# Kernel tuning notes

Hardware: AMD Instinct MI355X
Metric: run time of the kernel (lower is better)

The kernel has to match this reference:

```python
import jax, jax.numpy as jnp
import numpy as np

D = 1024   # embedding_dim
H = 16     # head_num
DH = D // H
STD = 0.02


def setup_inputs() -> dict:
    key = jax.random.key(0)
    ks = jax.random.split(key, 8)
    B, S = 16, 2048
    inp = {
        "hidden_states": jax.random.normal(ks[0], (B, S, D), dtype=jnp.float32),
        "attention_mask": jnp.zeros((B, 1, S), dtype=jnp.float32),
        # nn.Linear params, stored as [in, out] for direct matmul
        "Wq": jax.random.normal(ks[1], (D, D), dtype=jnp.float32) * STD,
        "bq": jnp.zeros((D,), dtype=jnp.float32),
        "Wqa": jax.random.normal(ks[2], (D, H), dtype=jnp.float32) * STD,
        "bqa": jnp.zeros((H,), dtype=jnp.float32),
        "Wk": jax.random.normal(ks[3], (D, D), dtype=jnp.float32) * STD,
        "bk": jnp.zeros((D,), dtype=jnp.float32),
        "Wka": jax.random.normal(ks[4], (D, H), dtype=jnp.float32) * STD,
        "bka": jnp.zeros((H,), dtype=jnp.float32),
        "Wt": jax.random.normal(ks[5], (D, D), dtype=jnp.float32) * STD,
        "bt": jnp.zeros((D,), dtype=jnp.float32),
    }
    return inp


def reference(hidden_states, attention_mask, Wq, bq, Wqa, bqa, Wk, bk, Wka, bka, Wt, bt):
    B, S, _ = hidden_states.shape
    scale = 1.0 / np.sqrt(DH).astype(np.float32)

    mixed_q = hidden_states @ Wq + bq          # [B,S,D]
    mixed_k = hidden_states @ Wk + bk          # [B,S,D]

    # per-head query pooling scores: [B,S,H] -> [B,H,S]
    q_score = jnp.transpose(mixed_q @ Wqa + bqa, (0, 2, 1)) * scale + attention_mask
    q_weight = jax.nn.softmax(q_score, axis=-1)                 # [B,H,S]

    q_layer = mixed_q.reshape(B, S, H, DH).transpose(0, 2, 1, 3)  # [B,H,S,dh]
    pooled_q = jnp.einsum('bhs,bhsd->bhd', q_weight, q_layer)     # [B,H,dh]
    pooled_q_flat = pooled_q.reshape(B, 1, D)                     # [B,1,D] (head-major)

    # elementwise modulate keys with pooled query (broadcast, no repeat)
    mixed_qk = mixed_k * pooled_q_flat                            # [B,S,D]

    qk_score = jnp.transpose(mixed_qk @ Wka + bka, (0, 2, 1)) * scale + attention_mask
    qk_weight = jax.nn.softmax(qk_score, axis=-1)                 # [B,H,S]

    k_layer = mixed_qk.reshape(B, S, H, DH).transpose(0, 2, 1, 3)  # [B,H,S,dh]
    pooled_k = jnp.einsum('bhs,bhsd->bhd', qk_weight, k_layer)     # [B,H,dh]

    weighted = pooled_k[:, :, None, :] * q_layer                   # [B,H,S,dh]
    weighted = weighted.transpose(0, 2, 1, 3).reshape(B, S, D)     # [B,S,D]

    return weighted @ Wt + bt + mixed_q
```

## Files before the change

### kernel.cpp

```cpp
#include <hip/hip_runtime.h>
#include <hip/hip_bf16.h>
#include <stdint.h>

#define D_ 1024
#define H_ 16
#define DH_ 64
#define S_ 2048
#define B_ 16
static constexpr float SCALE = 0.125f;

typedef __bf16 bf16_t;
typedef __bf16 bf16x8 __attribute__((ext_vector_type(8)));
typedef __bf16 bf16x4 __attribute__((ext_vector_type(4)));
typedef float  f32x4  __attribute__((ext_vector_type(4)));

__device__ __forceinline__ void llds16(const void* g, void* l) {
  __builtin_amdgcn_global_load_lds(
      (const __attribute__((address_space(1))) void*)g,
      (__attribute__((address_space(3))) void*)l, 16, 0, 0);
}

__global__ __launch_bounds__(256)
void prep_all(const float* __restrict__ Wq, const float* __restrict__ Wk,
              const float* __restrict__ Wt, const float* __restrict__ Wqa,
              const float* __restrict__ Wka, const float* __restrict__ hs,
              bf16_t* __restrict__ WqT, bf16_t* __restrict__ WkT,
              bf16_t* __restrict__ WtT, bf16_t* __restrict__ WqaT,
              bf16_t* __restrict__ WkaT, bf16_t* __restrict__ hsb) {
  __shared__ bf16_t t[64][65];
  const int z = blockIdx.z;
  const int tid = threadIdx.x;
  if (z < 3) {
    const float* src = (z == 0) ? Wq : (z == 1) ? Wk : Wt;
    bf16_t* dst      = (z == 0) ? WqT : (z == 1) ? WkT : WtT;
    const int n0 = blockIdx.x * 64, k0 = blockIdx.y * 64;
    const int r = tid >> 4, c4 = (tid & 15) * 4;
#pragma unroll
    for (int p = 0; p < 4; ++p) {
      int row = p * 16 + r;
      f32x4 f = *(const f32x4*)&src[(size_t)(k0 + row) * 1024 + n0 + c4];
#pragma unroll
      for (int i = 0; i < 4; ++i) t[row][c4 + i] = (bf16_t)f[i];
    }
    __syncthreads();
#pragma unroll
    for (int p = 0; p < 4; ++p) {
      int row = p * 16 + r;
      bf16x4 v;
#pragma unroll
      for (int i = 0; i < 4; ++i) v[i] = t[c4 + i][row];
      *(bf16x4*)&dst[(size_t)(n0 + row) * 1024 + k0 + c4] = v;
    }
  } else if (z == 3) {
    int g = (blockIdx.y * 16 + blockIdx.x) * 256 + tid;
    if (g < 2048) {
      const float* src = (g < 1024) ? Wqa : Wka;
      bf16_t* dst      = (g < 1024) ? WqaT : WkaT;
      int k = g & 1023;
#pragma unroll
      for (int h = 0; h < H_; ++h) dst[h * 1024 + k] = (bf16_t)src[k * H_ + h];
    }
  } else {
    const int slice = z - 4;
    const int fb = blockIdx.y * 16 + blockIdx.x;
    const size_t tbase = ((size_t)slice * 256 + fb) * 256 + tid;
#pragma unroll
    for (int i = 0; i < 4; ++i) {
      size_t e = (tbase + (size_t)i * 1048576) * 8;
      f32x4 a = *(const f32x4*)&hs[e];
      f32x4 b = *(const f32x4*)&hs[e + 4];
      bf16x8 o;
#pragma unroll
      for (int j = 0; j < 4; ++j) { o[j] = (bf16_t)a[j]; o[4 + j] = (bf16_t)b[j]; }
      *(bf16x8*)&hsb[e] = o;
    }
  }
}

__global__ __launch_bounds__(512, 1)
void gemm_qk(const bf16_t* __restrict__ A, const bf16_t* __restrict__ WqT,
             const bf16_t* __restrict__ WkT, const float* __restrict__ bq,
             const float* __restrict__ bk, bf16_t* __restrict__ mq,
             bf16_t* __restrict__ mk) {
  constexpr int K = 1024, N = 1024;
  __shared__ __align__(16) bf16_t lds[2][2][2][256 * 32];
  const int tid = threadIdx.x;
  const int lane = tid & 63, wid = tid >> 6;
  const int wm = wid >> 2, wn = wid & 3;

  const int wgid = (blockIdx.x & 7) * 128 + (blockIdx.x >> 3);
  const int m0 = (wgid >> 3) * 256;
  const int nsel = wgid & 7;
  const int n0 = (nsel & 3) * 256;
  const bf16_t* BT = (nsel < 4) ? WqT : WkT;
  const float* bias = (nsel < 4) ? bq : bk;
  bf16_t* Cout = (nsel < 4) ? mq : mk;

  int srow[2], scol[2];
#pragma unroll
  for (int ld = 0; ld < 2; ++ld) {
    int c = ld * 512 + tid;
    srow[ld] = c >> 2;
    scol[ld] = (((c & 3) - (srow[ld] & 3)) & 3) * 8;
  }

  const int ar = lane & 15;
  const int kc = lane >> 4;

  f32x4 acc[8][4] = {};

#define STAGE_(MAT, KH, KOFF, NXT)                                             \
  {                                                                            \
    const bf16_t* srcb = (MAT == 0) ? A : BT;                                  \
    const int rb = (MAT == 0) ? m0 : n0;                                       \
    _Pragma("unroll")                                                          \
    for (int ld = 0; ld < 2; ++ld) {                                           \
      llds16(srcb + (size_t)(rb + srow[ld]) * K + (KOFF) + (KH) * 32 + scol[ld], \
             &lds[NXT][MAT][KH][(ld * 512 + tid) * 8]);                        \
    }                                                                          \
  }

#define COMPUTE_(KH, MH, CUR)                                                  \
  {                                                                            \
    bf16x8 af[4], bg[4];                                                       \
    _Pragma("unroll")                                                          \
    for (int mm = 0; mm < 4; ++mm) {                                           \
      int r = wm * 128 + ((MH) * 4 + mm) * 16 + ar;                            \
      int slot = (kc + (r & 3)) & 3;                                           \
      af[mm] = *(const bf16x8*)&lds[CUR][0][KH][r * 32 + slot * 8];            \
    }                                                                          \
    _Pragma("unroll")                                                          \
    for (int nn = 0; nn < 4; ++nn) {                                           \
      int r = wn * 64 + nn * 16 + ar;                                          \
      int slot = (kc + (r & 3)) & 3;                                           \
      bg[nn] = *(const bf16x8*)&lds[CUR][1][KH][r * 32 + slot * 8];            \
    }                                                                          \
    __builtin_amdgcn_s_setprio(1);                                             \
    _Pragma("unroll")                                                          \
    for (int mm = 0; mm < 4; ++mm)                                             \
      _Pragma("unroll")                                                        \
      for (int nn = 0; nn < 4; ++nn)                                           \
        acc[(MH) * 4 + mm][nn] = __builtin_amdgcn_mfma_f32_16x16x32_bf16(      \
            af[mm], bg[nn], acc[(MH) * 4 + mm][nn], 0, 0, 0);                  \
    __builtin_amdgcn_s_setprio(0);                                             \
  }

  STAGE_(0, 0, 0, 0); STAGE_(1, 0, 0, 0); STAGE_(0, 1, 0, 0); STAGE_(1, 1, 0, 0);

#pragma unroll 1
  for (int t = 0; t < 15; ++t) {
    const int cur = t & 1, nxt = cur ^ 1;
    const int koff = (t + 1) * 64;
    STAGE_(0, 0, koff, nxt);
    asm volatile("s_waitcnt vmcnt(6)" ::: "memory");
    __builtin_amdgcn_s_barrier();
    COMPUTE_(0, 0, cur);
    STAGE_(1, 0, koff, nxt);
    COMPUTE_(0, 1, cur);
    STAGE_(0, 1, koff, nxt);
    asm volatile("s_waitcnt vmcnt(6)" ::: "memory");
    __builtin_amdgcn_s_barrier();
    COMPUTE_(1, 0, cur);
    STAGE_(1, 1, koff, nxt);
    COMPUTE_(1, 1, cur);
  }
  asm volatile("s_waitcnt vmcnt(4)" ::: "memory");
  __builtin_amdgcn_s_barrier();
  COMPUTE_(0, 0, 1);
  COMPUTE_(0, 1, 1);
  asm volatile("s_waitcnt vmcnt(0)" ::: "memory");
  __builtin_amdgcn_s_barrier();
  COMPUTE_(1, 0, 1);
  COMPUTE_(1, 1, 1);
#undef STAGE_
#undef COMPUTE_

  __syncthreads();

  float* st = (float*)&lds[0][0][0][0] + wid * (16 * 68);
  const int erow = lane >> 2;
  const int ecol = (lane & 3) * 16;
  const int gcb = n0 + wn * 64;
  const int qrow = (lane >> 4) * 4;
  const int qcol = lane & 15;
  f32x4 bb[4];
#pragma unroll
  for (int q = 0; q < 4; ++q) bb[q] = *(const f32x4*)&bias[gcb + ecol + q * 4];
#pragma unroll
  for (int m = 0; m < 8; ++m) {
#pragma unroll
    for (int n = 0; n < 4; ++n)
#pragma unroll
      for (int j = 0; j < 4; ++j)
        st[(qrow + j) * 68 + n * 16 + qcol] = acc[m][n][j];
    asm volatile("s_waitcnt lgkmcnt(0)" ::: "memory");
    __builtin_amdgcn_sched_barrier(0);
    const int grow = m0 + wm * 128 + m * 16 + erow;
    f32x4 v[4];
#pragma unroll
    for (int q = 0; q < 4; ++q) v[q] = *(f32x4*)&st[erow * 68 + ecol + q * 4];
#pragma unroll
    for (int q = 0; q < 4; ++q)
#pragma unroll
      for (int i = 0; i < 4; ++i) v[q][i] += bb[q][i];
    bf16x8 o0, o1;
#pragma unroll
    for (int i = 0; i < 4; ++i) { o0[i] = (bf16_t)v[0][i]; o0[4 + i] = (bf16_t)v[1][i]; }
#pragma unroll
    for (int i = 0; i < 4; ++i) { o1[i] = (bf16_t)v[2][i]; o1[4 + i] = (bf16_t)v[3][i]; }
    bf16_t* op = Cout + (size_t)grow * N + gcb + ecol;
    *(bf16x8*)&op[0] = o0;
    *(bf16x8*)&op[8] = o1;
  }
}

__global__ __launch_bounds__(256, 2)
void gemm_out(const bf16_t* __restrict__ A, const bf16_t* __restrict__ BT,
              const float* __restrict__ bias, float* __restrict__ Cout,
              const bf16_t* __restrict__ resid, const float* __restrict__ pkA) {
  constexpr int K = 1024, N = 1024;
  __shared__ __align__(16) bf16_t lA[128 * 32];
  __shared__ __align__(16) bf16_t lB[128 * 32];
  __shared__ __align__(16) float est[4][16 * 68];
  const int tid = threadIdx.x;
  const int lane = tid & 63, wid = tid >> 6;
  const int wr = wid >> 1, wc = wid & 1;

  const int wgid = (blockIdx.x & 7) * 256 + (blockIdx.x >> 3);
  const int m0 = (wgid >> 3) * 128;
  const int n0 = (wgid & 7) * 128;
  const int b = m0 / S_;

  const int ar = lane & 15;
  const int kq = lane >> 4;

  int rowc[2], colc[2], dstoff[2];
#pragma unroll
  for (int j = 0; j < 2; ++j) {
    int c = j * 256 + tid;
    int row = c >> 2, s = c & 3;
    rowc[j] = row;
    colc[j] = (((s - (row >> 1)) & 3) << 3);
    dstoff[j] = c * 8;
  }

  f32x4 acc[4][4] = {};

  for (int k0 = 0; k0 < K; k0 += 32) {
#pragma unroll
    for (int j = 0; j < 2; ++j) {
      llds16(BT + (size_t)(n0 + rowc[j]) * K + k0 + colc[j], lB + dstoff[j]);
      bf16x8 v = *(const bf16x8*)(A + (size_t)(m0 + rowc[j]) * K + k0 + colc[j]);
      const float* pkp = pkA + b * D_ + k0 + colc[j];
      f32x4 p0 = *(const f32x4*)pkp;
      f32x4 p1 = *(const f32x4*)(pkp + 4);
      bf16x8 o;
#pragma unroll
      for (int i = 0; i < 4; ++i) {
        o[i]     = (bf16_t)((float)v[i] * p0[i]);
        o[4 + i] = (bf16_t)((float)v[4 + i] * p1[i]);
      }
      *(bf16x8*)&lA[dstoff[j]] = o;
    }
    __syncthreads();
    bf16x8 af[4], bg[4];
#pragma unroll
    for (int m = 0; m < 4; ++m) {
      int r = wr * 64 + m * 16 + ar;
      af[m] = *(const bf16x8*)&lA[r * 32 + (((kq + (r >> 1)) & 3) << 3)];
    }
#pragma unroll
    for (int n = 0; n < 4; ++n) {
      int r = wc * 64 + n * 16 + ar;
      bg[n] = *(const bf16x8*)&lB[r * 32 + (((kq + (r >> 1)) & 3) << 3)];
    }
#pragma unroll
    for (int m = 0; m < 4; ++m)
#pragma unroll
      for (int n = 0; n < 4; ++n)
        acc[m][n] = __builtin_amdgcn_mfma_f32_16x16x32_bf16(af[m], bg[n], acc[m][n], 0, 0, 0);
    __syncthreads();
  }

  float* st = est[wid];
  const int erow = lane >> 2;
  const int ecol = (lane & 3) * 16;
  const int gcb = n0 + wc * 64;
  const int qrow = (lane >> 4) * 4;
  const int qcol = lane & 15;
  f32x4 bb[4];
#pragma unroll
  for (int q = 0; q < 4; ++q) bb[q] = *(const f32x4*)&bias[gcb + ecol + q * 4];
#pragma unroll
  for (int m = 0; m < 4; ++m) {
#pragma unroll
    for (int n = 0; n < 4; ++n)
#pragma unroll
      for (int j = 0; j < 4; ++j)
        st[(qrow + j) * 68 + n * 16 + qcol] = acc[m][n][j];
    asm volatile("s_waitcnt lgkmcnt(0)" ::: "memory");
    __builtin_amdgcn_sched_barrier(0);
    const int grow = m0 + wr * 64 + m * 16 + erow;
    f32x4 v[4];
#pragma unroll
    for (int q = 0; q < 4; ++q) v[q] = *(f32x4*)&st[erow * 68 + ecol + q * 4];
#pragma unroll
    for (int q = 0; q < 4; ++q)
#pragma unroll
      for (int i = 0; i < 4; ++i) v[q][i] += bb[q][i];
    bf16x8 r0 = *(const bf16x8*)&resid[(size_t)grow * N + gcb + ecol];
    bf16x8 r1 = *(const bf16x8*)&resid[(size_t)grow * N + gcb + ecol + 8];
#pragma unroll
    for (int i = 0; i < 4; ++i) { v[0][i] += (float)r0[i]; v[1][i] += (float)r0[4 + i]; }
#pragma unroll
    for (int i = 0; i < 4; ++i) { v[2][i] += (float)r1[i]; v[3][i] += (float)r1[4 + i]; }
    float* op = Cout + (size_t)grow * N + gcb + ecol;
#pragma unroll
    for (int q = 0; q < 4; ++q) *(f32x4*)&op[q * 4] = v[q];
  }
}

template <int PER_B>
__global__ __launch_bounds__(256)
void score_kernel(const bf16_t* __restrict__ X, const bf16_t* __restrict__ WaT,
                  const float* __restrict__ ba, const float* __restrict__ mask,
                  float* __restrict__ scores) {
  const int lane = threadIdx.x & 63, wid = threadIdx.x >> 6;
  const int m0 = blockIdx.x * 64 + wid * 16;
  const int ar = lane & 15, ak = (lane >> 4) * 8;
  const int bb = m0 >> 11;
  const bf16_t* Wb = WaT + (PER_B ? (size_t)bb * H_ * D_ : 0);
  f32x4 acc = {};
  for (int k0 = 0; k0 < D_; k0 += 32) {
    bf16x8 a = *(const bf16x8*)&X[(size_t)(m0 + ar) * D_ + k0 + ak];
    bf16x8 b = *(const bf16x8*)&Wb[(size_t)ar * D_ + k0 + ak];
    acc = __builtin_amdgcn_mfma_f32_16x16x32_bf16(a, b, acc, 0, 0, 0);
  }
  const int h = lane & 15;
  const int srow = m0 + (lane >> 4) * 4;
  const int s0 = srow - bb * S_;
  const float bah = ba[h];
  f32x4 mv = *(const f32x4*)&mask[(size_t)bb * S_ + s0];
  f32x4 outv;
#pragma unroll
  for (int j = 0; j < 4; ++j)
    outv[j] = (acc[j] + bah) * SCALE + mv[j];
  *(f32x4*)&scores[((size_t)(bb * H_ + h)) * S_ + s0] = outv;
}

__global__ __launch_bounds__(256)
void softmax_rows(const float* __restrict__ scores, float* __restrict__ wout) {
  __shared__ float rA[4], rB[4];
  const int tid = threadIdx.x, lane = tid & 63, wid = tid >> 6;
  const float* srow = scores + (size_t)blockIdx.x * S_;
  float* wrow = wout + (size_t)blockIdx.x * S_;
  f32x4 v0 = *(const f32x4*)&srow[tid * 4];
  f32x4 v1 = *(const f32x4*)&srow[1024 + tid * 4];
  float mx = fmaxf(fmaxf(fmaxf(v0[0], v0[1]), fmaxf(v0[2], v0[3])),
                   fmaxf(fmaxf(v1[0], v1[1]), fmaxf(v1[2], v1[3])));
#pragma unroll
  for (int o = 32; o; o >>= 1) mx = fmaxf(mx, __shfl_xor(mx, o));
  if (lane == 0) rA[wid] = mx;
  __syncthreads();
  mx = fmaxf(fmaxf(rA[0], rA[1]), fmaxf(rA[2], rA[3]));
  float sum = 0.f;
#pragma unroll
  for (int i = 0; i < 4; ++i) { v0[i] = __expf(v0[i] - mx); sum += v0[i]; }
#pragma unroll
  for (int i = 0; i < 4; ++i) { v1[i] = __expf(v1[i] - mx); sum += v1[i]; }
#pragma unroll
  for (int o = 32; o; o >>= 1) sum += __shfl_xor(sum, o);
  if (lane == 0) rB[wid] = sum;
  __syncthreads();
  sum = rB[0] + rB[1] + rB[2] + rB[3];
  const float inv = 1.0f / sum;
#pragma unroll
  for (int i = 0; i < 4; ++i) { v0[i] *= inv; v1[i] *= inv; }
  *(f32x4*)&wrow[tid * 4] = v0;
  *(f32x4*)&wrow[1024 + tid * 4] = v1;
}

__global__ __launch_bounds__(256)
void pool_partial(const bf16_t* __restrict__ X, const float* __restrict__ w,
                  float* __restrict__ partials) {
  __shared__ float sm[2][1024];
  const int tid = threadIdx.x;
  const int chunk = blockIdx.x, b = blockIdx.y;
  const int s0 = chunk * 32;
  const int dc = (tid & 127) * 8;
  const int sp = tid >> 7;
  const int h = dc >> 6;
  const float* wrow = w + ((size_t)b * H_ + h) * S_ + s0;
  const bf16_t* Xb = X + ((size_t)b * S_ + s0) * D_ + dc;
  float acc[8] = {};
  for (int s = sp; s < 32; s += 2) {
    bf16x8 xv = *(const bf16x8*)&Xb[(size_t)s * D_];
    float wt = wrow[s];
#pragma unroll
    for (int j = 0; j < 8; ++j) acc[j] += wt * (float)xv[j];
  }
#pragma unroll
  for (int j = 0; j < 8; ++j) sm[sp][dc + j] = acc[j];
  __syncthreads();
  const int d0 = tid * 4;
  f32x4 r;
#pragma unroll
  for (int j = 0; j < 4; ++j) r[j] = sm[0][d0 + j] + sm[1][d0 + j];
  *(f32x4*)&partials[((size_t)chunk * B_ + b) * D_ + d0] = r;
}

template <int MODE>
__global__ __launch_bounds__(256)
void pool_reduce(const float* __restrict__ partials, const float* __restrict__ pq,
                 const bf16_t* __restrict__ WkaT, float* __restrict__ pooled,
                 bf16_t* __restrict__ wka_s) {
  const int idx = blockIdx.x * 256 + threadIdx.x;
  float s = 0.f;
#pragma unroll 8
  for (int c = 0; c < 64; ++c) s += partials[(size_t)c * (B_ * D_) + idx];
  if (MODE == 1) s *= pq[idx];
  pooled[idx] = s;
  if (MODE == 0) {
    const int b = idx >> 10, d = idx & 1023;
#pragma unroll
    for (int h = 0; h < H_; ++h)
      wka_s[((size_t)b * H_ + h) * D_ + d] = (bf16_t)(s * (float)WkaT[h * D_ + d]);
  }
}

extern "C" void kernel_launch(void* const* d_in, const int* in_sizes, int n_in,
                              void* d_out, int out_size, void* d_ws, size_t ws_size,
                              hipStream_t stream) {
  const float* hs   = (const float*)d_in[0];
  const float* mask = (const float*)d_in[1];
  const float* Wq   = (const float*)d_in[2];
  const float* bq   = (const float*)d_in[3];
  const float* Wqa  = (const float*)d_in[4];
  const float* bqa  = (const float*)d_in[5];
  const float* Wk   = (const float*)d_in[6];
  const float* bk   = (const float*)d_in[7];
  const float* Wka  = (const float*)d_in[8];
  const float* bka  = (const float*)d_in[9];
  const float* Wt   = (const float*)d_in[10];
  const float* bt   = (const float*)d_in[11];

  char* ws = (char*)d_ws;
  float*  pq    = (float*)(ws + (64u << 10));
  float*  pk    = (float*)(ws + (128u << 10));
  bf16_t* wka_s = (bf16_t*)(ws + (256u << 10));
  bf16_t* WqaT  = (bf16_t*)(ws + (1u << 20));
  bf16_t* WkaT  = (bf16_t*)(ws + (1u << 20) + 32768);
  bf16_t* WqT   = (bf16_t*)(ws + (2u << 20));
  bf16_t* WkT   = (bf16_t*)(ws + (4u << 20));
  bf16_t* WtT   = (bf16_t*)(ws + (6u << 20));
  bf16_t* hsb   = (bf16_t*)(ws + (8u << 20));
  bf16_t* mq    = (bf16_t*)(ws + (8u << 20) + ((size_t)64 << 20));
  bf16_t* mk    = (bf16_t*)(ws + (8u << 20) + ((size_t)128 << 20));
  float* scores = (float*)(ws + (8u << 20) + ((size_t)192 << 20));
  float* wsm    = (float*)(ws + (8u << 20) + ((size_t)194 << 20));
  float* parts  = (float*)(ws + (8u << 20) + ((size_t)196 << 20));

  prep_all<<<dim3(16, 16, 20), 256, 0, stream>>>(Wq, Wk, Wt, Wqa, Wka, hs,
                                                 WqT, WkT, WtT, WqaT, WkaT, hsb);

  gemm_qk<<<1024, 512, 0, stream>>>(hsb, WqT, WkT, bq, bk, mq, mk);

  score_kernel<0><<<512, 256, 0, stream>>>(mq, WqaT, bqa, mask, scores);
  softmax_rows<<<256, 256, 0, stream>>>(scores, wsm);
  pool_partial<<<dim3(64, 16), 256, 0, stream>>>(mq, wsm, parts);
  pool_reduce<0><<<64, 256, 0, stream>>>(parts, nullptr, WkaT, pq, wka_s);

  score_kernel<1><<<512, 256, 0, stream>>>(mk, wka_s, bka, mask, scores);
  softmax_rows<<<256, 256, 0, stream>>>(scores, wsm);
  pool_partial<<<dim3(64, 16), 256, 0, stream>>>(mk, wsm, parts);
  pool_reduce<1><<<64, 256, 0, stream>>>(parts, pq, nullptr, pk, nullptr);

  gemm_out<<<2048, 256, 0, stream>>>(mq, WtT, bt, (float*)d_out, mq, pk);
}
```

Before: 365.4 us.

## Fold pooled-key scaling into per-batch Wt copies and use pipelined 256x256 GEMM

Instead of scaling the A operand (mq) by pk inside the output GEMM's load loop, a new kernel builds a per-batch copy of WtT with pk folded into its K dimension. The output GEMM then becomes a plain GEMM using the same 256x256-tile, 512-thread, double-buffered global_load_lds pipeline as the QK projection. The LDS swizzle in gemm_qk is also changed to use (row>>1). The cost is 32 MB of extra weight traffic and one more launch, traded for removing register-path loads and the per-element multiply from the GEMM mainloop.

```diff
diff --git a/kernel.cpp b/kernel.cpp
--- a/kernel.cpp
+++ b/kernel.cpp
@@ -101,7 +101,7 @@
   for (int ld = 0; ld < 2; ++ld) {
     int c = ld * 512 + tid;
     srow[ld] = c >> 2;
-    scol[ld] = (((c & 3) - (srow[ld] & 3)) & 3) * 8;
+    scol[ld] = (((c & 3) - ((srow[ld] >> 1) & 3)) & 3) * 8;
   }
 
   const int ar = lane & 15;
@@ -126,13 +126,13 @@
     _Pragma("unroll")                                                          \
     for (int mm = 0; mm < 4; ++mm) {                                           \
       int r = wm * 128 + ((MH) * 4 + mm) * 16 + ar;                            \
-      int slot = (kc + (r & 3)) & 3;                                           \
+      int slot = (kc + ((r >> 1) & 3)) & 3;                                    \
       af[mm] = *(const bf16x8*)&lds[CUR][0][KH][r * 32 + slot * 8];            \
     }                                                                          \
     _Pragma("unroll")                                                          \
     for (int nn = 0; nn < 4; ++nn) {                                           \
       int r = wn * 64 + nn * 16 + ar;                                          \
-      int slot = (kc + (r & 3)) & 3;                                           \
+      int slot = (kc + ((r >> 1) & 3)) & 3;                                    \
       bg[nn] = *(const bf16x8*)&lds[CUR][1][KH][r * 32 + slot * 8];            \
     }                                                                          \
     __builtin_amdgcn_s_setprio(1);                                             \
@@ -214,85 +214,133 @@
   }
 }
 
-__global__ __launch_bounds__(256, 2)
-void gemm_out(const bf16_t* __restrict__ A, const bf16_t* __restrict__ BT,
-              const float* __restrict__ bias, float* __restrict__ Cout,
-              const bf16_t* __restrict__ resid, const float* __restrict__ pkA) {
+__global__ __launch_bounds__(256)
+void wt_scale(const bf16_t* __restrict__ WtT, const float* __restrict__ pk,
+              bf16_t* __restrict__ wt_s) {
+  size_t e = ((size_t)blockIdx.x * 256 + threadIdx.x) * 8;
+  const int b = (int)(e >> 20);
+  const int nk = (int)(e & 1048575);
+  const int k = nk & 1023;
+  bf16x8 w = *(const bf16x8*)&WtT[nk];
+  const float* pp = &pk[b * D_ + k];
+  f32x4 p0 = *(const f32x4*)pp;
+  f32x4 p1 = *(const f32x4*)(pp + 4);
+  bf16x8 o;
+#pragma unroll
+  for (int i = 0; i < 4; ++i) {
+    o[i]     = (bf16_t)((float)w[i] * p0[i]);
+    o[4 + i] = (bf16_t)((float)w[4 + i] * p1[i]);
+  }
+  *(bf16x8*)&wt_s[e] = o;
+}
+
+__global__ __launch_bounds__(512, 1)
+void gemm_out8(const bf16_t* __restrict__ A, const bf16_t* __restrict__ WtS,
+               const float* __restrict__ bias, float* __restrict__ Cout,
+               const bf16_t* __restrict__ resid) {
   constexpr int K = 1024, N = 1024;
-  __shared__ __align__(16) bf16_t lA[128 * 32];
-  __shared__ __align__(16) bf16_t lB[128 * 32];
-  __shared__ __align__(16) float est[4][16 * 68];
+  __shared__ __align__(16) bf16_t lds[2][2][2][256 * 32];
   const int tid = threadIdx.x;
   const int lane = tid & 63, wid = tid >> 6;
-  const int wr = wid >> 1, wc = wid & 1;
-
-  const int wgid = (blockIdx.x & 7) * 256 + (blockIdx.x >> 3);
-  const int m0 = (wgid >> 3) * 128;
-  const int n0 = (wgid & 7) * 128;
-  const int b = m0 / S_;
+  const int wm = wid >> 2, wn = wid & 3;
+
+  const int wgid = (blockIdx.x & 7) * 64 + (blockIdx.x >> 3);
+  const int m0 = (wgid >> 2) * 256;
+  const int n0 = (wgid & 3) * 256;
+  const bf16_t* BT = WtS + ((size_t)(m0 >> 11) << 20);
+
+  int srow[2], scol[2];
+#pragma unroll
+  for (int ld = 0; ld < 2; ++ld) {
+    int c = ld * 512 + tid;
+    srow[ld] = c >> 2;
+    scol[ld] = (((c & 3) - ((srow[ld] >> 1) & 3)) & 3) * 8;
+  }
 
   const int ar = lane & 15;
-  const int kq = lane >> 4;
-
-  int rowc[2], colc[2], dstoff[2];
-#pragma unroll
-  for (int j = 0; j < 2; ++j) {
-    int c = j * 256 + tid;
-    int row = c >> 2, s = c & 3;
-    rowc[j] = row;
-    colc[j] = (((s - (row >> 1)) & 3) << 3);
-    dstoff[j] = c * 8;
-  }
-
-  f32x4 acc[4][4] = {};
-
-  for (int k0 = 0; k0 < K; k0 += 32) {
-#pragma unroll
-    for (int j = 0; j < 2; ++j) {
-      llds16(BT + (size_t)(n0 + rowc[j]) * K + k0 + colc[j], lB + dstoff[j]);
-      bf16x8 v = *(const bf16x8*)(A + (size_t)(m0 + rowc[j]) * K + k0 + colc[j]);
-      const float* pkp = pkA + b * D_ + k0 + colc[j];
-      f32x4 p0 = *(const f32x4*)pkp;
-      f32x4 p1 = *(const f32x4*)(pkp + 4);
-      bf16x8 o;
-#pragma unroll
-      for (int i = 0; i < 4; ++i) {
-        o[i]     = (bf16_t)((float)v[i] * p0[i]);
-        o[4 + i] = (bf16_t)((float)v[4 + i] * p1[i]);
-      }
-      *(bf16x8*)&lA[dstoff[j]] = o;
-    }
-    __syncthreads();
-    bf16x8 af[4], bg[4];
-#pragma unroll
-    for (int m = 0; m < 4; ++m) {
-      int r = wr * 64 + m * 16 + ar;
-      af[m] = *(const bf16x8*)&lA[r * 32 + (((kq + (r >> 1)) & 3) << 3)];
-    }
-#pragma unroll
-    for (int n = 0; n < 4; ++n) {
-      int r = wc * 64 + n * 16 + ar;
-      bg[n] = *(const bf16x8*)&lB[r * 32 + (((kq + (r >> 1)) & 3) << 3)];
-    }
-#pragma unroll
-    for (int m = 0; m < 4; ++m)
-#pragma unroll
-      for (int n = 0; n < 4; ++n)
-        acc[m][n] = __builtin_amdgcn_mfma_f32_16x16x32_bf16(af[m], bg[n], acc[m][n], 0, 0, 0);
-    __syncthreads();
-  }
-
-  float* st = est[wid];
+  const int kc = lane >> 4;
+
+  f32x4 acc[8][4] = {};
+
+#define STAGE2_(MAT, KH, KOFF, NXT)                                            \
+  {                                                                            \
+    const bf16_t* srcb = (MAT == 0) ? A : BT;                                  \
+    const int rb = (MAT == 0) ? m0 : n0;                                       \
+    _Pragma("unroll")                                                          \
+    for (int ld = 0; ld < 2; ++ld) {                                           \
+      llds16(srcb + (size_t)(rb + srow[ld]) * K + (KOFF) + (KH) * 32 + scol[ld], \
+             &lds[NXT][MAT][KH][(ld * 512 + tid) * 8]);                        \
+    }                                                                          \
+  }
+
+#define COMPUTE2_(KH, MH, CUR)                                                 \
+  {                                                                            \
+    bf16x8 af[4], bg[4];                                                       \
+    _Pragma("unroll")                                                          \
+    for (int mm = 0; mm < 4; ++mm) {                                           \
+      int r = wm * 128 + ((MH) * 4 + mm) * 16 + ar;                            \
+      int slot = (kc + ((r >> 1) & 3)) & 3;                                    \
+      af[mm] = *(const bf16x8*)&lds[CUR][0][KH][r * 32 + slot * 8];            \
+    }                                                                          \
+    _Pragma("unroll")                                                          \
+    for (int nn = 0; nn < 4; ++nn) {                                           \
+      int r = wn * 64 + nn * 16 + ar;                                          \
+      int slot = (kc + ((r >> 1) & 3)) & 3;                                    \
+      bg[nn] = *(const bf16x8*)&lds[CUR][1][KH][r * 32 + slot * 8];            \
+    }                                                                          \
+    __builtin_amdgcn_s_setprio(1);                                             \
+    _Pragma("unroll")                                                          \
+    for (int mm = 0; mm < 4; ++mm)                                             \
+      _Pragma("unroll")                                                        \
+      for (int nn = 0; nn < 4; ++nn)                                           \
+        acc[(MH) * 4 + mm][nn] = __builtin_amdgcn_mfma_f32_16x16x32_bf16(      \
+            af[mm], bg[nn], acc[(MH) * 4 + mm][nn], 0, 0, 0);                  \
+    __builtin_amdgcn_s_setprio(0);                                             \
+  }
+
+  STAGE2_(0, 0, 0, 0); STAGE2_(1, 0, 0, 0); STAGE2_(0, 1, 0, 0); STAGE2_(1, 1, 0, 0);
+
+#pragma unroll 1
+  for (int t = 0; t < 15; ++t) {
+    const int cur = t & 1, nxt = cur ^ 1;
+    const int koff = (t + 1) * 64;
+    STAGE2_(0, 0, koff, nxt);
+    asm volatile("s_waitcnt vmcnt(6)" ::: "memory");
+    __builtin_amdgcn_s_barrier();
+    COMPUTE2_(0, 0, cur);
+    STAGE2_(1, 0, koff, nxt);
+    COMPUTE2_(0, 1, cur);
+    STAGE2_(0, 1, koff, nxt);
+    asm volatile("s_waitcnt vmcnt(6)" ::: "memory");
+    __builtin_amdgcn_s_barrier();
+    COMPUTE2_(1, 0, cur);
+    STAGE2_(1, 1, koff, nxt);
+    COMPUTE2_(1, 1, cur);
+  }
+  asm volatile("s_waitcnt vmcnt(4)" ::: "memory");
+  __builtin_amdgcn_s_barrier();
+  COMPUTE2_(0, 0, 1);
+  COMPUTE2_(0, 1, 1);
+  asm volatile("s_waitcnt vmcnt(0)" ::: "memory");
+  __builtin_amdgcn_s_barrier();
+  COMPUTE2_(1, 0, 1);
+  COMPUTE2_(1, 1, 1);
+#undef STAGE2_
+#undef COMPUTE2_
+
+  __syncthreads();
+
+  float* st = (float*)&lds[0][0][0][0] + wid * (16 * 68);
   const int erow = lane >> 2;
   const int ecol = (lane & 3) * 16;
-  const int gcb = n0 + wc * 64;
+  const int gcb = n0 + wn * 64;
   const int qrow = (lane >> 4) * 4;
   const int qcol = lane & 15;
   f32x4 bb[4];
 #pragma unroll
   for (int q = 0; q < 4; ++q) bb[q] = *(const f32x4*)&bias[gcb + ecol + q * 4];
 #pragma unroll
-  for (int m = 0; m < 4; ++m) {
+  for (int m = 0; m < 8; ++m) {
 #pragma unroll
     for (int n = 0; n < 4; ++n)
 #pragma unroll
@@ -300,7 +348,7 @@
         st[(qrow + j) * 68 + n * 16 + qcol] = acc[m][n][j];
     asm volatile("s_waitcnt lgkmcnt(0)" ::: "memory");
     __builtin_amdgcn_sched_barrier(0);
-    const int grow = m0 + wr * 64 + m * 16 + erow;
+    const int grow = m0 + wm * 128 + m * 16 + erow;
     f32x4 v[4];
 #pragma unroll
     for (int q = 0; q < 4; ++q) v[q] = *(f32x4*)&st[erow * 68 + ecol + q * 4];
@@ -459,6 +507,7 @@
   float* scores = (float*)(ws + (8u << 20) + ((size_t)192 << 20));
   float* wsm    = (float*)(ws + (8u << 20) + ((size_t)194 << 20));
   float* parts  = (float*)(ws + (8u << 20) + ((size_t)196 << 20));
+  bf16_t* wt_s  = (bf16_t*)(ws + (8u << 20) + ((size_t)208 << 20));
 
   prep_all<<<dim3(16, 16, 20), 256, 0, stream>>>(Wq, Wk, Wt, Wqa, Wka, hs,
                                                  WqT, WkT, WtT, WqaT, WkaT, hsb);
@@ -475,5 +524,6 @@
   pool_partial<<<dim3(64, 16), 256, 0, stream>>>(mk, wsm, parts);
   pool_reduce<1><<<64, 256, 0, stream>>>(parts, pq, nullptr, pk, nullptr);
 
-  gemm_out<<<2048, 256, 0, stream>>>(mq, WtT, bt, (float*)d_out, mq, pk);
-}
+  wt_scale<<<8192, 256, 0, stream>>>(WtT, pk, wt_s);
+  gemm_out8<<<512, 512, 0, stream>>>(mq, wt_s, bt, (float*)d_out, mq);
+}
```

Result: faster. 357.4 us (-2.2%).
